# Performance work log

Measured on AMD Instinct MI355X. Metric: run time of the kernel, lower is better.

The kernel has to match this reference:

```python
import jax, jax.numpy as jnp
import numpy as np

B, H, W, C = 32, 256, 256, 32

def setup_inputs() -> dict:
    key = jax.random.key(0)
    inputs = jax.random.normal(key, (B, H, W, C), dtype=jnp.float32)
    return {"inputs": inputs}

def reference(inputs) -> jnp.ndarray:
    # Space-to-depth into an 8x8 grid of cells.
    # Original: split H into 8 row-bands, W into 8 col-bands, flatten each
    # (H/8, W/8, C) cell row-major. Equivalent to reshape + transpose + reshape.
    b, h, w, c = inputs.shape
    hh, ww = h // 8, w // 8
    x = inputs.reshape(b, 8, hh, 8, ww, c)          # (B, 8, H/8, 8, W/8, C)
    x = x.transpose(0, 1, 3, 2, 4, 5)               # (B, 8, 8, H/8, W/8, C)
    return x.reshape(b, 8, 8, hh * ww * c)          # (B, 8, 8, H*W*C/64)
```

## Files before the change

### kernel.cpp

```cpp
#include <hip/hip_runtime.h>


__global__ __launch_bounds__(256) void chessboard_kernel(
    const float4* __restrict__ in, float4* __restrict__ out) {
    unsigned g      = blockIdx.x * 256u + threadIdx.x;
    unsigned within = g & 255u;
    unsigned blk    = g >> 8;

    unsigned r = blk & 31u;
    unsigned j = (blk >> 5) & 7u;
    unsigned i = (blk >> 8) & 7u;
    unsigned b = blk >> 11;

    unsigned in_blk = (b * 256u + i * 32u + r) * 8u + j;
    out[g] = in[in_blk * 256u + within];
}

extern "C" void kernel_launch(void* const* d_in, const int* in_sizes, int n_in,
                              void* d_out, int out_size, void* d_ws, size_t ws_size,
                              hipStream_t stream) {
    const float4* in  = (const float4*)d_in[0];
    float4*       out = (float4*)d_out;
    chessboard_kernel<<<65536, 256, 0, stream>>>(in, out);
}
```

Baseline: 425.7 us.

## Use grid-stride loop with four nontemporal vector copies per thread

```diff
diff --git a/kernel.cpp b/kernel.cpp
--- a/kernel.cpp
+++ b/kernel.cpp
@@ -1,25 +1,36 @@
 #include <hip/hip_runtime.h>
 
 
+typedef float f32x4 __attribute__((ext_vector_type(4)));
+
 __global__ __launch_bounds__(256) void chessboard_kernel(
-    const float4* __restrict__ in, float4* __restrict__ out) {
-    unsigned g      = blockIdx.x * 256u + threadIdx.x;
-    unsigned within = g & 255u;
-    unsigned blk    = g >> 8;
+    const f32x4* __restrict__ in, f32x4* __restrict__ out) {
+    const unsigned t = threadIdx.x;
+    for (unsigned gq = blockIdx.x; gq < 16384u; gq += gridDim.x) {
+        unsigned r0 = (gq & 7u) * 4u;
+        unsigned j  = (gq >> 3) & 7u;
+        unsigned i  = (gq >> 6) & 7u;
+        unsigned b  = gq >> 9;
 
-    unsigned r = blk & 31u;
-    unsigned j = (blk >> 5) & 7u;
-    unsigned i = (blk >> 8) & 7u;
-    unsigned b = blk >> 11;
+        unsigned in_base  = ((b * 256u + i * 32u + r0) * 8u + j) * 256u + t;
+        unsigned out_base = gq * 1024u + t;
 
-    unsigned in_blk = (b * 256u + i * 32u + r) * 8u + j;
-    out[g] = in[in_blk * 256u + within];
+        f32x4 v0 = __builtin_nontemporal_load(&in[in_base]);
+        f32x4 v1 = __builtin_nontemporal_load(&in[in_base + 2048u]);
+        f32x4 v2 = __builtin_nontemporal_load(&in[in_base + 4096u]);
+        f32x4 v3 = __builtin_nontemporal_load(&in[in_base + 6144u]);
+
+        __builtin_nontemporal_store(v0, &out[out_base]);
+        __builtin_nontemporal_store(v1, &out[out_base + 256u]);
+        __builtin_nontemporal_store(v2, &out[out_base + 512u]);
+        __builtin_nontemporal_store(v3, &out[out_base + 768u]);
+    }
 }
 
 extern "C" void kernel_launch(void* const* d_in, const int* in_sizes, int n_in,
                               void* d_out, int out_size, void* d_ws, size_t ws_size,
                               hipStream_t stream) {
-    const float4* in  = (const float4*)d_in[0];
-    float4*       out = (float4*)d_out;
-    chessboard_kernel<<<65536, 256, 0, stream>>>(in, out);
+    const f32x4* in  = (const f32x4*)d_in[0];
+    f32x4*       out = (f32x4*)d_out;
+    chessboard_kernel<<<2048, 256, 0, stream>>>(in, out);
 }
```

After: 417.1 us. 1.02x faster.
